# Kernel tuning notes

Measured on AMD Instinct MI355X. Metric: run time of the kernel, lower is better.

The kernel has to match this reference:

```python
import jax, jax.numpy as jnp
import numpy as np

GROUPS = 256   # B: number of index groups
SEQ = 512      # L: tokens per group (equal-length groups)
D_IN = 128
D_QK = 64
D_V = 128


def setup_inputs() -> dict:
    key = jax.random.key(0)
    ks = jax.random.split(key, 7)
    N = GROUPS * SEQ
    inputs = jax.random.normal(ks[0], (N, D_IN), dtype=jnp.float32)
    # sorted group ids: GROUPS groups of SEQ tokens each
    index = jnp.repeat(jnp.arange(GROUPS, dtype=jnp.int64), SEQ)
    s_in = 1.0 / np.sqrt(D_IN)
    Wq = jax.random.normal(ks[1], (D_IN, D_QK), dtype=jnp.float32) * s_in
    bq = jax.random.normal(ks[2], (D_QK,), dtype=jnp.float32) * 0.01
    Wk = jax.random.normal(ks[3], (D_IN, D_QK), dtype=jnp.float32) * s_in
    bk = jax.random.normal(ks[4], (D_QK,), dtype=jnp.float32) * 0.01
    Wv = jax.random.normal(ks[5], (D_IN, D_V), dtype=jnp.float32) * s_in
    bv = jax.random.normal(ks[6], (D_V,), dtype=jnp.float32) * 0.01
    return {"inputs": inputs, "index": index, "Wq": Wq, "bq": bq,
            "Wk": Wk, "bk": bk, "Wv": Wv, "bv": bv}


def reference(inputs, index, Wq, bq, Wk, bk, Wv, bv):
    # Linear projections on flat tokens [N, d]
    q = inputs @ Wq + bq          # [N, D_QK]
    k = inputs @ Wk + bk          # [N, D_QK]
    v = inputs @ Wv + bv          # [N, D_V]
    # unbatch: equal-length sorted groups -> [B, L, d]
    q = q.reshape(GROUPS, SEQ, D_QK)
    k = k.reshape(GROUPS, SEQ, D_QK)
    v = v.reshape(GROUPS, SEQ, D_V)
    # note the module's scale: sqrt(2 * d_qk)
    scale = 1.0 / np.sqrt(2.0 * D_QK).astype(np.float32)
    scores = jnp.einsum('bqd,bkd->bqk', q, k) * scale   # [B, L, L]
    attn = jax.nn.softmax(scores, axis=-1)
    out = jnp.einsum('bqk,bkd->bqd', attn, v)           # [B, L, D_V]
    return out.reshape(-1, D_V)                          # [N, D_V]
```

## Files before the change

### kernel.cpp

```cpp
#include <hip/hip_runtime.h>
#include <hip/hip_bf16.h>
#include <stdint.h>

#define GROUPS 256
#define SEQ    512
#define D_IN   128
#define D_QK   64
#define D_V    128
#define NTOK   (GROUPS * SEQ)

#define SL2E (0.08838834764831845f * 1.4426950408889634f)

typedef short bf8 __attribute__((ext_vector_type(8)));
typedef short bf4 __attribute__((ext_vector_type(4)));
typedef float f32x4 __attribute__((ext_vector_type(4)));

__device__ __forceinline__ short f2bf(float f) {
    __bf16 h = (__bf16)f;
    return __builtin_bit_cast(short, h);
}

__device__ __forceinline__ void gload_lds16(const void* g, void* l) {
    __builtin_amdgcn_global_load_lds(
        (const __attribute__((address_space(1))) unsigned int*)(uintptr_t)(g),
        (__attribute__((address_space(3))) unsigned int*)(uint32_t)(uintptr_t)(l),
        16, 0, 0);
}

__global__ __launch_bounds__(256) void prep_w(
    const float* __restrict__ Wq, const float* __restrict__ bq,
    const float* __restrict__ Wk, const float* __restrict__ bk,
    const float* __restrict__ Wv, const float* __restrict__ bv,
    short* __restrict__ Wt, float* __restrict__ bcat)
{
    const int t = blockIdx.x * 256 + threadIdx.x;
    const int r  = t >> 5;
    const int k0 = (t & 31) * 4;
    const float* W; int ld; int c; float sc;
    if (r < 64)       { W = Wq; ld = 64;  c = r;       sc = SL2E; }
    else if (r < 128) { W = Wk; ld = 64;  c = r - 64;  sc = 1.0f; }
    else              { W = Wv; ld = 128; c = r - 128; sc = 1.0f; }
    bf4 pk;
#pragma unroll
    for (int i = 0; i < 4; ++i) pk[i] = f2bf(W[(size_t)(k0 + i) * ld + c] * sc);
    const int phys = (k0 * 2) ^ ((r & 7) << 4);
    *reinterpret_cast<bf4*>((char*)Wt + r * 256 + phys) = pk;
    if (t < 256) {
        const float* b = (t < 64) ? bq : (t < 128 ? bk : bv);
        const int cb   = (t < 64) ? t  : (t < 128 ? t - 64 : t - 128);
        bcat[t] = b[cb] * (t < 64 ? SL2E : 1.0f);
    }
}

__global__ __launch_bounds__(256) void proj_kernel(
    const float* __restrict__ x, const short* __restrict__ Wt,
    const float* __restrict__ bcat,
    short* __restrict__ Q, short* __restrict__ K, short* __restrict__ Vt)
{
    __shared__ short wlds[32768];
    const int tid = threadIdx.x;
    const int wid = tid >> 6, lane = tid & 63, l15 = lane & 15, lg = lane >> 4;

#pragma unroll
    for (int i = 0; i < 16; ++i)
        gload_lds16((const char*)Wt + i * 4096 + tid * 16,
                    (char*)wlds + i * 4096 + tid * 16);

    const size_t tw = (size_t)blockIdx.x * 256 + wid * 64;
    const int g     = (int)(tw >> 9);
    const int tseg  = (int)(tw & 511);

    bf8 xf[4][4];
#pragma unroll
    for (int m = 0; m < 4; ++m) {
        const float* xr = x + (tw + m * 16 + l15) * D_IN;
#pragma unroll
        for (int kf = 0; kf < 4; ++kf) {
            const float4 a = *reinterpret_cast<const float4*>(xr + kf * 32 + lg * 8);
            const float4 b = *reinterpret_cast<const float4*>(xr + kf * 32 + lg * 8 + 4);
            bf8 v;
            v[0] = f2bf(a.x); v[1] = f2bf(a.y); v[2] = f2bf(a.z); v[3] = f2bf(a.w);
            v[4] = f2bf(b.x); v[5] = f2bf(b.y); v[6] = f2bf(b.z); v[7] = f2bf(b.w);
            xf[m][kf] = v;
        }
    }
    __syncthreads();

#pragma unroll
    for (int cf = 0; cf < 16; ++cf) {
        const int wrow = cf * 16 + l15;
        bf8 wf[4];
#pragma unroll
        for (int kf = 0; kf < 4; ++kf) {
            const int off = (kf * 64 + lg * 16) ^ ((wrow & 7) << 4);
            wf[kf] = *reinterpret_cast<const bf8*>((const char*)wlds + wrow * 256 + off);
        }

        if (cf < 8) {
            const float4 bias4 = *reinterpret_cast<const float4*>(bcat + cf * 16 + lg * 4);
#pragma unroll
            for (int m = 0; m < 4; ++m) {
                f32x4 acc = (f32x4){0.f, 0.f, 0.f, 0.f};
#pragma unroll
                for (int kf = 0; kf < 4; ++kf)
                    acc = __builtin_amdgcn_mfma_f32_16x16x32_bf16(wf[kf], xf[m][kf], acc, 0, 0, 0);
                bf4 pk;
                pk[0] = f2bf(acc[0] + bias4.x); pk[1] = f2bf(acc[1] + bias4.y);
                pk[2] = f2bf(acc[2] + bias4.z); pk[3] = f2bf(acc[3] + bias4.w);
                const size_t tok = tw + m * 16 + l15;
                if (cf < 4) {
                    *reinterpret_cast<bf4*>((char*)Q + tok * 128 + cf * 32 + lg * 8) = pk;
                } else {
                    const int lo = ((cf - 4) * 32 + lg * 8) ^ (((int)tok & 7) << 4);
                    *reinterpret_cast<bf4*>((char*)K + tok * 128 + lo) = pk;
                }
            }
        } else {
            const int d = (cf - 8) * 16 + l15;
            const float bias = bcat[cf * 16 + l15];
            char* vrow = (char*)Vt + (((size_t)g * D_V + d) << 10);
#pragma unroll
            for (int m = 0; m < 4; ++m) {
                f32x4 acc = (f32x4){0.f, 0.f, 0.f, 0.f};
#pragma unroll
                for (int kf = 0; kf < 4; ++kf)
                    acc = __builtin_amdgcn_mfma_f32_16x16x32_bf16(xf[m][kf], wf[kf], acc, 0, 0, 0);
                bf4 pk;
#pragma unroll
                for (int r = 0; r < 4; ++r) pk[r] = f2bf(acc[r] + bias);
                const int t0    = tseg + m * 16;
                const int blk32 = t0 >> 5;
                const int half  = (t0 >> 4) & 1;
                const int logi  = blk32 * 64 + lg * 16 + half * 8;
                const int phys  = (logi & ~127) | ((logi & 127) ^ ((d & 7) << 4));
                *reinterpret_cast<bf4*>(vrow + phys) = pk;
            }
        }
    }
}

__global__ __launch_bounds__(256, 3) void attn_kernel(
    const short* __restrict__ Q, const short* __restrict__ K,
    const short* __restrict__ Vt, float* __restrict__ out)
{
    __shared__ short lds[2 * 12288];
    const int g = blockIdx.x, rb = blockIdx.y;
    const int tid = threadIdx.x, wid = tid >> 6, lane = tid & 63;
    const int l15 = lane & 15, lg = lane >> 4;
    const size_t gtok = (size_t)g * SEQ;
    const int row0 = rb * 128 + wid * 32;

    bf8 qf[2][2];
#pragma unroll
    for (int rf = 0; rf < 2; ++rf) {
        const short* qr = Q + (gtok + row0 + rf * 16 + l15) * 64 + lg * 8;
        qf[rf][0] = *reinterpret_cast<const bf8*>(qr);
        qf[rf][1] = *reinterpret_cast<const bf8*>(qr + 32);
    }

    const char* Kg = (const char*)(K + gtok * 64);
    const char* Vg = (const char*)(Vt + ((size_t)g * D_V << 9));

    f32x4 o[2][8];
#pragma unroll
    for (int rf = 0; rf < 2; ++rf)
#pragma unroll
        for (int vt = 0; vt < 8; ++vt) o[rf][vt] = (f32x4){0.f, 0.f, 0.f, 0.f};
    f32x4 psv[2] = {(f32x4){0.f, 0.f, 0.f, 0.f}, (f32x4){0.f, 0.f, 0.f, 0.f}};
    const bf8 onesf = {0x3F80, 0x3F80, 0x3F80, 0x3F80, 0x3F80, 0x3F80, 0x3F80, 0x3F80};

    auto stage = [&](int kt, int b) {
        char* lbase = (char*)lds + b * 24576;
        int c = wid * 6;
#pragma unroll
        for (int i = 0; i < 6; ++i, ++c) {
            if (c < 8) {
                gload_lds16(Kg + (size_t)kt * 8192 + c * 1024 + lane * 16,
                            lbase + c * 1024 + lane * 16);
            } else {
                const int cv = c - 8;
                const int d  = cv * 8 + (lane >> 3);
                gload_lds16(Vg + (size_t)d * 1024 + kt * 128 + (lane & 7) * 16,
                            lbase + 8192 + cv * 1024 + lane * 16);
            }
        }
    };

    auto compute = [&](int b) {
        const char* lb = (const char*)lds + b * 24576;
        f32x4 st[4][2];
#pragma unroll
        for (int tf = 0; tf < 4; ++tf) {
            const int tok = tf * 16 + l15;
            const char* kb = lb + tok * 128;
            const int x7 = (tok & 7) << 4;
            const bf8 k0 = *reinterpret_cast<const bf8*>(kb + ((lg * 16) ^ x7));
            const bf8 k1 = *reinterpret_cast<const bf8*>(kb + ((64 + lg * 16) ^ x7));
#pragma unroll
            for (int rf = 0; rf < 2; ++rf) {
                f32x4 s = (f32x4){0.f, 0.f, 0.f, 0.f};
                s = __builtin_amdgcn_mfma_f32_16x16x32_bf16(k0, qf[rf][0], s, 0, 0, 0);
                s = __builtin_amdgcn_mfma_f32_16x16x32_bf16(k1, qf[rf][1], s, 0, 0, 0);
                st[tf][rf] = s;
            }
        }
        bf8 pa[2][2];
#pragma unroll
        for (int rf = 0; rf < 2; ++rf) {
#pragma unroll
            for (int ks = 0; ks < 2; ++ks) {
                bf8 pv;
#pragma unroll
                for (int i = 0; i < 4; ++i) {
                    pv[i]     = f2bf(__builtin_amdgcn_exp2f(st[2 * ks][rf][i]));
                    pv[i + 4] = f2bf(__builtin_amdgcn_exp2f(st[2 * ks + 1][rf][i]));
                }
                pa[rf][ks] = pv;
                psv[rf] = __builtin_amdgcn_mfma_f32_16x16x32_bf16(pv, onesf, psv[rf], 0, 0, 0);
            }
        }
        const char* vb = lb + 8192;
#pragma unroll
        for (int vt = 0; vt < 8; ++vt) {
            const int d = vt * 16 + l15;
            const char* vr = vb + d * 128;
            const int x7 = (d & 7) << 4;
            const bf8 v0 = *reinterpret_cast<const bf8*>(vr + ((lg * 16) ^ x7));
            const bf8 v1 = *reinterpret_cast<const bf8*>(vr + ((64 + lg * 16) ^ x7));
            o[0][vt] = __builtin_amdgcn_mfma_f32_16x16x32_bf16(pa[0][0], v0, o[0][vt], 0, 0, 0);
            o[1][vt] = __builtin_amdgcn_mfma_f32_16x16x32_bf16(pa[1][0], v0, o[1][vt], 0, 0, 0);
            o[0][vt] = __builtin_amdgcn_mfma_f32_16x16x32_bf16(pa[0][1], v1, o[0][vt], 0, 0, 0);
            o[1][vt] = __builtin_amdgcn_mfma_f32_16x16x32_bf16(pa[1][1], v1, o[1][vt], 0, 0, 0);
        }
    };

    stage(0, 0);
    stage(1, 1);
#pragma unroll 1
    for (int kt = 0; kt < 8; ++kt) {
        const int b = kt & 1;
        if (kt < 7) { asm volatile("s_waitcnt vmcnt(6)" ::: "memory"); }
        else        { asm volatile("s_waitcnt vmcnt(0)" ::: "memory"); }
        __builtin_amdgcn_s_barrier();
        asm volatile("" ::: "memory");
        compute(b);
        if (kt + 2 < 8) {
            asm volatile("" ::: "memory");
            __builtin_amdgcn_s_barrier();
            stage(kt + 2, b);
        }
    }

#pragma unroll
    for (int rf = 0; rf < 2; ++rf) {
        float linv[4];
#pragma unroll
        for (int r = 0; r < 4; ++r) linv[r] = 1.0f / psv[rf][r];
        float* op = out + (gtok + row0 + rf * 16) * D_V;
#pragma unroll
        for (int vt = 0; vt < 8; ++vt)
#pragma unroll
            for (int r = 0; r < 4; ++r)
                op[(size_t)(lg * 4 + r) * D_V + vt * 16 + l15] = o[rf][vt][r] * linv[r];
    }
}

extern "C" void kernel_launch(void* const* d_in, const int* in_sizes, int n_in,
                              void* d_out, int out_size, void* d_ws, size_t ws_size,
                              hipStream_t stream) {
    (void)in_sizes; (void)n_in; (void)ws_size; (void)out_size;
    const float* x  = (const float*)d_in[0];
    const float* Wq = (const float*)d_in[2];
    const float* bq = (const float*)d_in[3];
    const float* Wk = (const float*)d_in[4];
    const float* bk = (const float*)d_in[5];
    const float* Wv = (const float*)d_in[6];
    const float* bv = (const float*)d_in[7];
    float* out = (float*)d_out;

    short* Qw = (short*)d_ws;
    short* Kw = Qw + (size_t)NTOK * D_QK;
    short* Vt = Kw + (size_t)NTOK * D_QK;

    short* Wt   = (short*)out;
    float* bcat = (float*)((char*)out + 65536);

    prep_w<<<32, 256, 0, stream>>>(Wq, bq, Wk, bk, Wv, bv, Wt, bcat);
    proj_kernel<<<NTOK / 256, 256, 0, stream>>>(x, Wt, bcat, Qw, Kw, Vt);
    attn_kernel<<<dim3(GROUPS, 4), 256, 0, stream>>>(Qw, Kw, Vt, out);
}
```

Measured before the change: 75.81 us.

## Halve attention key tile to 32 tokens and raise occupancy to four blocks

```diff
diff --git a/kernel.cpp b/kernel.cpp
--- a/kernel.cpp
+++ b/kernel.cpp
@@ -119,6 +119,7 @@
             const int d = (cf - 8) * 16 + l15;
             const float bias = bcat[cf * 16 + l15];
             char* vrow = (char*)Vt + (((size_t)g * D_V + d) << 10);
+            const int sd = (d >> 1) & 3;
 #pragma unroll
             for (int m = 0; m < 4; ++m) {
                 f32x4 acc = (f32x4){0.f, 0.f, 0.f, 0.f};
@@ -128,22 +129,19 @@
                 bf4 pk;
 #pragma unroll
                 for (int r = 0; r < 4; ++r) pk[r] = f2bf(acc[r] + bias);
-                const int t0    = tseg + m * 16;
-                const int blk32 = t0 >> 5;
-                const int half  = (t0 >> 4) & 1;
-                const int logi  = blk32 * 64 + lg * 16 + half * 8;
-                const int phys  = (logi & ~127) | ((logi & 127) ^ ((d & 7) << 4));
+                const int t0   = tseg + m * 16;
+                const int phys = (t0 >> 5) * 64 + ((lg ^ sd) << 4) + ((t0 >> 4) & 1) * 8;
                 *reinterpret_cast<bf4*>(vrow + phys) = pk;
             }
         }
     }
 }
 
-__global__ __launch_bounds__(256, 3) void attn_kernel(
+__global__ __launch_bounds__(256, 4) void attn_kernel(
     const short* __restrict__ Q, const short* __restrict__ K,
     const short* __restrict__ Vt, float* __restrict__ out)
 {
-    __shared__ short lds[2 * 12288];
+    __shared__ short lds[2 * 6144];
     const int g = blockIdx.x, rb = blockIdx.y;
     const int tid = threadIdx.x, wid = tid >> 6, lane = tid & 63;
     const int l15 = lane & 15, lg = lane >> 4;
@@ -170,27 +168,27 @@
     const bf8 onesf = {0x3F80, 0x3F80, 0x3F80, 0x3F80, 0x3F80, 0x3F80, 0x3F80, 0x3F80};
 
     auto stage = [&](int kt, int b) {
-        char* lbase = (char*)lds + b * 24576;
-        int c = wid * 6;
-#pragma unroll
-        for (int i = 0; i < 6; ++i, ++c) {
-            if (c < 8) {
-                gload_lds16(Kg + (size_t)kt * 8192 + c * 1024 + lane * 16,
+        char* lbase = (char*)lds + b * 12288;
+        int c = wid * 3;
+#pragma unroll
+        for (int i = 0; i < 3; ++i, ++c) {
+            if (c < 4) {
+                gload_lds16(Kg + (size_t)kt * 4096 + c * 1024 + lane * 16,
                             lbase + c * 1024 + lane * 16);
             } else {
-                const int cv = c - 8;
-                const int d  = cv * 8 + (lane >> 3);
-                gload_lds16(Vg + (size_t)d * 1024 + kt * 128 + (lane & 7) * 16,
-                            lbase + 8192 + cv * 1024 + lane * 16);
+                const int cv = c - 4;
+                const int d  = cv * 16 + (lane >> 2);
+                gload_lds16(Vg + (size_t)d * 1024 + kt * 64 + (lane & 3) * 16,
+                            lbase + 4096 + cv * 1024 + lane * 16);
             }
         }
     };
 
     auto compute = [&](int b) {
-        const char* lb = (const char*)lds + b * 24576;
-        f32x4 st[4][2];
-#pragma unroll
-        for (int tf = 0; tf < 4; ++tf) {
+        const char* lb = (const char*)lds + b * 12288;
+        f32x4 st[2][2];
+#pragma unroll
+        for (int tf = 0; tf < 2; ++tf) {
             const int tok = tf * 16 + l15;
             const char* kb = lb + tok * 128;
             const int x7 = (tok & 7) << 4;
@@ -204,51 +202,36 @@
                 st[tf][rf] = s;
             }
         }
-        bf8 pa[2][2];
+        bf8 pa[2];
 #pragma unroll
         for (int rf = 0; rf < 2; ++rf) {
-#pragma unroll
-            for (int ks = 0; ks < 2; ++ks) {
-                bf8 pv;
-#pragma unroll
-                for (int i = 0; i < 4; ++i) {
-                    pv[i]     = f2bf(__builtin_amdgcn_exp2f(st[2 * ks][rf][i]));
-                    pv[i + 4] = f2bf(__builtin_amdgcn_exp2f(st[2 * ks + 1][rf][i]));
-                }
-                pa[rf][ks] = pv;
-                psv[rf] = __builtin_amdgcn_mfma_f32_16x16x32_bf16(pv, onesf, psv[rf], 0, 0, 0);
-            }
-        }
-        const char* vb = lb + 8192;
+            bf8 pv;
+#pragma unroll
+            for (int i = 0; i < 4; ++i) {
+                pv[i]     = f2bf(__builtin_amdgcn_exp2f(st[0][rf][i]));
+                pv[i + 4] = f2bf(__builtin_amdgcn_exp2f(st[1][rf][i]));
+            }
+            pa[rf] = pv;
+            psv[rf] = __builtin_amdgcn_mfma_f32_16x16x32_bf16(pv, onesf, psv[rf], 0, 0, 0);
+        }
+        const char* vb = lb + 4096;
 #pragma unroll
         for (int vt = 0; vt < 8; ++vt) {
             const int d = vt * 16 + l15;
-            const char* vr = vb + d * 128;
-            const int x7 = (d & 7) << 4;
-            const bf8 v0 = *reinterpret_cast<const bf8*>(vr + ((lg * 16) ^ x7));
-            const bf8 v1 = *reinterpret_cast<const bf8*>(vr + ((64 + lg * 16) ^ x7));
-            o[0][vt] = __builtin_amdgcn_mfma_f32_16x16x32_bf16(pa[0][0], v0, o[0][vt], 0, 0, 0);
-            o[1][vt] = __builtin_amdgcn_mfma_f32_16x16x32_bf16(pa[1][0], v0, o[1][vt], 0, 0, 0);
-            o[0][vt] = __builtin_amdgcn_mfma_f32_16x16x32_bf16(pa[0][1], v1, o[0][vt], 0, 0, 0);
-            o[1][vt] = __builtin_amdgcn_mfma_f32_16x16x32_bf16(pa[1][1], v1, o[1][vt], 0, 0, 0);
+            const char* vr = vb + d * 64;
+            const bf8 v0 = *reinterpret_cast<const bf8*>(vr + ((lg * 16) ^ ((((d >> 1) & 3)) << 4)));
+            o[0][vt] = __builtin_amdgcn_mfma_f32_16x16x32_bf16(pa[0], v0, o[0][vt], 0, 0, 0);
+            o[1][vt] = __builtin_amdgcn_mfma_f32_16x16x32_bf16(pa[1], v0, o[1][vt], 0, 0, 0);
         }
     };
 
     stage(0, 0);
-    stage(1, 1);
-#pragma unroll 1
-    for (int kt = 0; kt < 8; ++kt) {
+    __syncthreads();
+    for (int kt = 0; kt < 16; ++kt) {
         const int b = kt & 1;
-        if (kt < 7) { asm volatile("s_waitcnt vmcnt(6)" ::: "memory"); }
-        else        { asm volatile("s_waitcnt vmcnt(0)" ::: "memory"); }
-        __builtin_amdgcn_s_barrier();
-        asm volatile("" ::: "memory");
+        if (kt < 15) stage(kt + 1, b ^ 1);
         compute(b);
-        if (kt + 2 < 8) {
-            asm volatile("" ::: "memory");
-            __builtin_amdgcn_s_barrier();
-            stage(kt + 2, b);
-        }
+        __syncthreads();
     }
 
 #pragma unroll
```

Result: no change. 75.60 us (-0.3%).
